# Optimization experiments

Measured on AMD Instinct MI355X. Metric: run time of the kernel, lower is better.

## Reference

```python
import jax, jax.numpy as jnp
import numpy as np

K_TOP = 2        # experts_per_tok
E_MLP = 8        # num_mlp_experts


def setup_inputs() -> dict:
    key = jax.random.key(0)
    ks = jax.random.split(key, 6)
    B, T, C, H, E_ve, V = 2, 2048, 1024, 2048, 2, 32000
    return {
        "x": jax.random.normal(ks[0], (B, T, C), dtype=jnp.float32),
        "token_ids": jax.random.randint(ks[1], (B, T), 0, V, dtype=jnp.int32),
        "w_up": jax.random.normal(ks[2], (E_MLP, H, C), dtype=jnp.float32) * 0.02,
        "w_down": jax.random.normal(ks[3], (E_MLP, C, H), dtype=jnp.float32) * 0.02,
        "router_w": jax.random.normal(ks[4], (E_MLP + E_ve, C), dtype=jnp.float32) * 0.02,
        "router_bias": jnp.zeros((E_MLP + E_ve,), dtype=jnp.float32),
        "ve_tables": jax.random.normal(ks[5], (E_ve, V, C), dtype=jnp.float32) * 0.02,
    }


def reference(x, token_ids, w_up, w_down, router_w, router_bias, ve_tables):
    B, T, C = x.shape
    N = B * T
    E_total = router_w.shape[0]
    x_flat = x.reshape(N, C)

    # Sigmoid router with aux-loss-free bias (DeepSeekV3 style): select top-k on
    # biased scores, gate with unbiased sigmoid scores normalized over the top-k.
    scores = jax.nn.sigmoid(x_flat @ router_w.T)              # (N, E_total)
    _, top_idx = jax.lax.top_k(scores + router_bias, K_TOP)   # (N, k)
    top_w = jnp.take_along_axis(scores, top_idx, axis=1)      # (N, k)
    top_w = top_w / jnp.sum(top_w, axis=1, keepdims=True)

    rows = jnp.arange(N)[:, None]
    sparse_w = jnp.zeros((N, E_total), dtype=x.dtype).at[rows, top_idx].set(top_w)

    # Dense all-expert FFN (relu^2 activation), then mask by routing weights.
    hidden = jnp.einsum('nc,ehc->enh', x_flat, w_up)          # (E_mlp, N, H)
    hidden = jnp.square(jax.nn.relu(hidden))
    mlp_out = jnp.einsum('enh,ech->enc', hidden, w_down)      # (E_mlp, N, C)
    mlp_contrib = jnp.einsum('enc,ne->nc', mlp_out, sparse_w[:, :E_MLP])

    # VE experts: shared embedding lookups, (E_ve, N, C).
    ve_out = ve_tables[:, token_ids.reshape(N), :]
    ve_contrib = jnp.einsum('enc,ne->nc', ve_out, sparse_w[:, E_MLP:])

    return (mlp_contrib + ve_contrib).reshape(B, T, C)
```

## Files before the change

kernel.cpp:

```cpp
#include <hip/hip_runtime.h>
#include <hip/hip_bf16.h>
#include <stdint.h>

#define N_TOK 4096
#define C_DIM 1024
#define H_DIM 2048
#define V_DIM 32000
#define NE_MLP 8
#define NE_TOT 10

typedef __attribute__((ext_vector_type(8))) short bf16x8;
typedef __attribute__((ext_vector_type(4))) short bf16x4;
typedef __attribute__((ext_vector_type(4))) float f32x4;

#define BM 128
#define BN 128
#define HKE 32
#define HALF_ELEMS (128 * 32)

__device__ __forceinline__ void gload16(const void* g, void* l) {
    __builtin_amdgcn_global_load_lds(
        (const __attribute__((address_space(1))) void*)g,
        (__attribute__((address_space(3))) void*)l,
        16, 0, 0);
}

__device__ __forceinline__ unsigned short bf16bits(float v) {
    __hip_bfloat16 h = __float2bfloat16(v);
    return *reinterpret_cast<unsigned short*>(&h);
}

#define CVT_N0 (N_TOK * C_DIM / 4)
#define CVT_N1 (NE_MLP * H_DIM * C_DIM / 4)
__global__ void __launch_bounds__(256) cvt_kernel(
    const float* __restrict__ x, const float* __restrict__ wu,
    const float* __restrict__ wd, __hip_bfloat16* __restrict__ xb,
    __hip_bfloat16* __restrict__ wub, __hip_bfloat16* __restrict__ wdb)
{
    const int i = blockIdx.x * 256 + threadIdx.x;
    const float* src;
    __hip_bfloat16* dst;
    int j;
    if (i < CVT_N0)            { src = x;  dst = xb;  j = i; }
    else if (i < CVT_N0 + CVT_N1) { src = wu; dst = wub; j = i - CVT_N0; }
    else                       { src = wd; dst = wdb; j = i - CVT_N0 - CVT_N1; }
    f32x4 v = reinterpret_cast<const f32x4*>(src)[j];
    bf16x4 b;
    b.x = (short)bf16bits(v.x); b.y = (short)bf16bits(v.y);
    b.z = (short)bf16bits(v.z); b.w = (short)bf16bits(v.w);
    reinterpret_cast<bf16x4*>(dst)[j] = b;
}

__global__ void __launch_bounds__(256) router_kernel(
    const float* __restrict__ x, const float* __restrict__ rw,
    const float* __restrict__ rb, int* __restrict__ tok_list,
    int* __restrict__ te, int* __restrict__ tp, float* __restrict__ tw,
    float* __restrict__ vw, int* __restrict__ cnt)
{
    const int lane = threadIdx.x & 63;
    const int n = blockIdx.x * 4 + (threadIdx.x >> 6);
    const f32x4* xr  = reinterpret_cast<const f32x4*>(x + (size_t)n * C_DIM);
    const f32x4* rw4 = reinterpret_cast<const f32x4*>(rw);

    float acc[NE_TOT];
    #pragma unroll
    for (int e = 0; e < NE_TOT; ++e) acc[e] = 0.f;

    #pragma unroll
    for (int kk = 0; kk < C_DIM / 256; ++kk) {
        f32x4 xv = xr[kk * 64 + lane];
        #pragma unroll
        for (int e = 0; e < NE_TOT; ++e) {
            f32x4 wv = rw4[e * (C_DIM / 4) + kk * 64 + lane];
            acc[e] += xv.x * wv.x + xv.y * wv.y + xv.z * wv.z + xv.w * wv.w;
        }
    }
    #pragma unroll
    for (int e = 0; e < NE_TOT; ++e) {
        for (int m = 32; m > 0; m >>= 1) acc[e] += __shfl_xor(acc[e], m, 64);
    }

    if (lane == 0) {
        float s[NE_TOT], sb[NE_TOT];
        #pragma unroll
        for (int e = 0; e < NE_TOT; ++e) {
            s[e]  = 1.f / (1.f + expf(-acc[e]));
            sb[e] = s[e] + rb[e];
        }
        int i0 = 0;
        #pragma unroll
        for (int e = 1; e < NE_TOT; ++e) if (sb[e] > sb[i0]) i0 = e;
        int i1 = (i0 == 0) ? 1 : 0;
        #pragma unroll
        for (int e = 0; e < NE_TOT; ++e)
            if (e != i0 && sb[e] > sb[i1]) i1 = e;

        float w0 = s[i0], w1 = s[i1];
        float inv = 1.f / (w0 + w1);
        w0 *= inv; w1 *= inv;

        float wv0 = 0.f, wv1 = 0.f;
        int   idx[2] = {i0, i1};
        float wt[2]  = {w0, w1};
        #pragma unroll
        for (int k = 0; k < 2; ++k) {
            if (idx[k] < NE_MLP) {
                int p = atomicAdd(&cnt[idx[k]], 1);
                tok_list[idx[k] * N_TOK + p] = n;
                te[n * 2 + k] = idx[k];
                tp[n * 2 + k] = p;
                tw[n * 2 + k] = wt[k];
            } else {
                te[n * 2 + k] = -1;
                tp[n * 2 + k] = 0;
                tw[n * 2 + k] = 0.f;
                if (idx[k] == NE_MLP) wv0 = wt[k]; else wv1 = wt[k];
            }
        }
        vw[n * 2 + 0] = wv0;
        vw[n * 2 + 1] = wv1;
    }
}

__global__ void __launch_bounds__(256) up_kernel(
    const __hip_bfloat16* __restrict__ xb, const __hip_bfloat16* __restrict__ wub,
    const int* __restrict__ tok_list, const int* __restrict__ cnt,
    __hip_bfloat16* __restrict__ hidden)
{
    const int e = blockIdx.z;
    const int count = cnt[e];
    const int m0 = blockIdx.y * BM;
    if (m0 >= count) return;
    const int n0 = blockIdx.x * BN;

    __shared__ __hip_bfloat16 lA[2 * HALF_ELEMS];
    __shared__ __hip_bfloat16 lB[2 * HALF_ELEMS];

    const int tid  = threadIdx.x;
    const int lane = tid & 63;
    const int wv   = tid >> 6;
    const int wm = (wv >> 1) * 64;
    const int wn = (wv & 1) * 64;

    const __hip_bfloat16* ga[2];
    const __hip_bfloat16* gb[2];
    __hip_bfloat16* la[2];
    __hip_bfloat16* lb[2];
    const __hip_bfloat16* wB = wub + (size_t)e * H_DIM * C_DIM;
    #pragma unroll
    for (int t = 0; t < 2; ++t) {
        const int srow = (wv + 4 * t) * 16 + (lane >> 2);
        int r = m0 + srow;
        const int tok = tok_list[e * N_TOK + (r < count ? r : count - 1)];
        ga[t] = xb + (size_t)tok * C_DIM + (lane & 3) * 8;
        gb[t] = wB + (size_t)(n0 + srow) * C_DIM + (lane & 3) * 8;
        la[t] = lA + (wv + 4 * t) * 512;
        lb[t] = lB + (wv + 4 * t) * 512;
    }

    f32x4 acc[4][4];
    #pragma unroll
    for (int i = 0; i < 4; ++i)
        #pragma unroll
        for (int j = 0; j < 4; ++j)
            acc[i][j] = (f32x4){0.f, 0.f, 0.f, 0.f};

    const int fm  = lane & 15;
    const int fkb = (lane >> 4) * 8;

    for (int k0 = 0; k0 < C_DIM; k0 += 2 * HKE) {
        __syncthreads();
        #pragma unroll
        for (int h = 0; h < 2; ++h) {
            #pragma unroll
            for (int t = 0; t < 2; ++t) {
                gload16(ga[t] + h * HKE, la[t] + h * HALF_ELEMS);
                gload16(gb[t] + h * HKE, lb[t] + h * HALF_ELEMS);
            }
        }
        #pragma unroll
        for (int t = 0; t < 2; ++t) { ga[t] += 2 * HKE; gb[t] += 2 * HKE; }
        __syncthreads();
        #pragma unroll
        for (int h = 0; h < 2; ++h) {
            bf16x8 af[4], bfr[4];
            #pragma unroll
            for (int i = 0; i < 4; ++i) {
                af[i]  = *reinterpret_cast<const bf16x8*>(lA + h * HALF_ELEMS + (wm + i * 16 + fm) * HKE + fkb);
                bfr[i] = *reinterpret_cast<const bf16x8*>(lB + h * HALF_ELEMS + (wn + i * 16 + fm) * HKE + fkb);
            }
            #pragma unroll
            for (int i = 0; i < 4; ++i)
                #pragma unroll
                for (int j = 0; j < 4; ++j)
                    acc[i][j] = __builtin_amdgcn_mfma_f32_16x16x32_bf16(af[i], bfr[j], acc[i][j], 0, 0, 0);
        }
    }

    const int fr = (lane >> 4) * 4;
    #pragma unroll
    for (int i = 0; i < 4; ++i) {
        #pragma unroll
        for (int r = 0; r < 4; ++r) {
            const int gr = m0 + wm + i * 16 + fr + r;
            const bool ok = gr < count;
            unsigned int pk[4];
            #pragma unroll
            for (int j = 0; j < 4; ++j) {
                float v = acc[i][j][r];
                v = v > 0.f ? v * v : 0.f;
                unsigned short b = bf16bits(v);
                int other = __shfl_xor((int)b, 1, 64);
                pk[j] = (unsigned)b | ((unsigned)other << 16);
            }
            if (ok && !(lane & 1)) {
                __hip_bfloat16* hrow = hidden + (size_t)(e * N_TOK + gr) * H_DIM + n0 + wn + fm;
                #pragma unroll
                for (int j = 0; j < 4; ++j)
                    *reinterpret_cast<unsigned int*>(hrow + j * 16) = pk[j];
            }
        }
    }
}

#define MLP_SLAB ((size_t)NE_MLP * N_TOK * C_DIM)
__global__ void __launch_bounds__(256) down_kernel(
    const __hip_bfloat16* __restrict__ hidden, const __hip_bfloat16* __restrict__ wdb,
    const int* __restrict__ cnt, float* __restrict__ mlp_buf)
{
    const int e  = blockIdx.z >> 1;
    const int kh = blockIdx.z & 1;
    const int count = cnt[e];
    const int m0 = blockIdx.y * BM;
    if (m0 >= count) return;
    const int n0 = blockIdx.x * BN;
    const int kbase = kh * (H_DIM / 2);

    __shared__ __hip_bfloat16 lA[2 * HALF_ELEMS];
    __shared__ __hip_bfloat16 lB[2 * HALF_ELEMS];

    const int tid  = threadIdx.x;
    const int lane = tid & 63;
    const int wv   = tid >> 6;
    const int wm = (wv >> 1) * 64;
    const int wn = (wv & 1) * 64;

    const __hip_bfloat16* ga[2];
    const __hip_bfloat16* gb[2];
    __hip_bfloat16* la[2];
    __hip_bfloat16* lb[2];
    const __hip_bfloat16* wB = wdb + (size_t)e * C_DIM * H_DIM;
    #pragma unroll
    for (int t = 0; t < 2; ++t) {
        const int srow = (wv + 4 * t) * 16 + (lane >> 2);
        int r = m0 + srow;
        const int arow = e * N_TOK + (r < count ? r : count - 1);
        ga[t] = hidden + (size_t)arow * H_DIM + kbase + (lane & 3) * 8;
        gb[t] = wB + (size_t)(n0 + srow) * H_DIM + kbase + (lane & 3) * 8;
        la[t] = lA + (wv + 4 * t) * 512;
        lb[t] = lB + (wv + 4 * t) * 512;
    }

    f32x4 acc[4][4];
    #pragma unroll
    for (int i = 0; i < 4; ++i)
        #pragma unroll
        for (int j = 0; j < 4; ++j)
            acc[i][j] = (f32x4){0.f, 0.f, 0.f, 0.f};

    const int fm  = lane & 15;
    const int fkb = (lane >> 4) * 8;

    for (int k0 = 0; k0 < H_DIM / 2; k0 += 2 * HKE) {
        __syncthreads();
        #pragma unroll
        for (int h = 0; h < 2; ++h) {
            #pragma unroll
            for (int t = 0; t < 2; ++t) {
                gload16(ga[t] + h * HKE, la[t] + h * HALF_ELEMS);
                gload16(gb[t] + h * HKE, lb[t] + h * HALF_ELEMS);
            }
        }
        #pragma unroll
        for (int t = 0; t < 2; ++t) { ga[t] += 2 * HKE; gb[t] += 2 * HKE; }
        __syncthreads();
        #pragma unroll
        for (int h = 0; h < 2; ++h) {
            bf16x8 af[4], bfr[4];
            #pragma unroll
            for (int i = 0; i < 4; ++i) {
                af[i]  = *reinterpret_cast<const bf16x8*>(lA + h * HALF_ELEMS + (wm + i * 16 + fm) * HKE + fkb);
                bfr[i] = *reinterpret_cast<const bf16x8*>(lB + h * HALF_ELEMS + (wn + i * 16 + fm) * HKE + fkb);
            }
            #pragma unroll
            for (int i = 0; i < 4; ++i)
                #pragma unroll
                for (int j = 0; j < 4; ++j)
                    acc[i][j] = __builtin_amdgcn_mfma_f32_16x16x32_bf16(af[i], bfr[j], acc[i][j], 0, 0, 0);
        }
    }

    float* obuf = mlp_buf + (size_t)kh * MLP_SLAB;
    const int fr = (lane >> 4) * 4;
    #pragma unroll
    for (int i = 0; i < 4; ++i) {
        #pragma unroll
        for (int r = 0; r < 4; ++r) {
            const int gr = m0 + wm + i * 16 + fr + r;
            if (gr < count) {
                float* orow = obuf + (size_t)(e * N_TOK + gr) * C_DIM + n0 + wn + fm;
                #pragma unroll
                for (int j = 0; j < 4; ++j)
                    orow[j * 16] = acc[i][j][r];
            }
        }
    }
}

__global__ void __launch_bounds__(256) combine_kernel(
    const int* __restrict__ token_ids, const float* __restrict__ vt,
    const float* __restrict__ vw, const int* __restrict__ te,
    const int* __restrict__ tp, const float* __restrict__ tw,
    const float* __restrict__ mlp_buf, float* __restrict__ out)
{
    const int n = blockIdx.x;
    const int c = threadIdx.x;
    const int t = token_ids[n];
    const float w0 = vw[n * 2 + 0];
    const float w1 = vw[n * 2 + 1];
    f32x4 v = {0.f, 0.f, 0.f, 0.f};
    if (w0 != 0.f)
        v += w0 * reinterpret_cast<const f32x4*>(vt + (size_t)t * C_DIM)[c];
    if (w1 != 0.f)
        v += w1 * reinterpret_cast<const f32x4*>(vt + ((size_t)V_DIM + t) * C_DIM)[c];
    #pragma unroll
    for (int k = 0; k < 2; ++k) {
        const int e = te[n * 2 + k];
        if (e >= 0) {
            const size_t slot = (size_t)(e * N_TOK + tp[n * 2 + k]) * C_DIM;
            f32x4 a = reinterpret_cast<const f32x4*>(mlp_buf + slot)[c];
            f32x4 b = reinterpret_cast<const f32x4*>(mlp_buf + MLP_SLAB + slot)[c];
            v += tw[n * 2 + k] * (a + b);
        }
    }
    reinterpret_cast<f32x4*>(out + (size_t)n * C_DIM)[c] = v;
}

extern "C" void kernel_launch(void* const* d_in, const int* in_sizes, int n_in,
                              void* d_out, int out_size, void* d_ws, size_t ws_size,
                              hipStream_t stream)
{
    const float* x         = (const float*)d_in[0];
    const int*   token_ids = (const int*)  d_in[1];
    const float* w_up      = (const float*)d_in[2];
    const float* w_down    = (const float*)d_in[3];
    const float* router_w  = (const float*)d_in[4];
    const float* router_b  = (const float*)d_in[5];
    const float* ve_tables = (const float*)d_in[6];
    float* out = (float*)d_out;

    char* ws = (char*)d_ws;
    size_t off = 0;
    __hip_bfloat16* hidden  = (__hip_bfloat16*)(ws + off); off += (size_t)NE_MLP * N_TOK * H_DIM * 2;
    float*          mlp_buf = (float*)         (ws + off); off += 2 * MLP_SLAB * 4;
    __hip_bfloat16* xb      = (__hip_bfloat16*)(ws + off); off += (size_t)N_TOK * C_DIM * 2;
    __hip_bfloat16* wub     = (__hip_bfloat16*)(ws + off); off += (size_t)NE_MLP * H_DIM * C_DIM * 2;
    __hip_bfloat16* wdb     = (__hip_bfloat16*)(ws + off); off += (size_t)NE_MLP * C_DIM * H_DIM * 2;
    int*   tok_list = (int*)  (ws + off); off += (size_t)NE_MLP * N_TOK * 4;
    int*   te       = (int*)  (ws + off); off += (size_t)N_TOK * 2 * 4;
    int*   tp       = (int*)  (ws + off); off += (size_t)N_TOK * 2 * 4;
    float* tw       = (float*)(ws + off); off += (size_t)N_TOK * 2 * 4;
    float* vw       = (float*)(ws + off); off += (size_t)N_TOK * 2 * 4;
    int*   cnt      = (int*)  (ws + off); off += 64;

    hipMemsetAsync(cnt, 0, NE_MLP * sizeof(int), stream);

    cvt_kernel<<<(CVT_N0 + 2 * CVT_N1) / 256, 256, 0, stream>>>(
        x, w_up, w_down, xb, wub, wdb);
    router_kernel<<<N_TOK / 4, 256, 0, stream>>>(x, router_w, router_b,
                                                 tok_list, te, tp, tw, vw, cnt);
    up_kernel<<<dim3(H_DIM / BN, N_TOK / BM, NE_MLP), 256, 0, stream>>>(
        xb, wub, tok_list, cnt, hidden);
    down_kernel<<<dim3(C_DIM / BN, N_TOK / BM, NE_MLP * 2), 256, 0, stream>>>(
        hidden, wdb, cnt, mlp_buf);
    combine_kernel<<<N_TOK, 256, 0, stream>>>(token_ids, ve_tables, vw,
                                              te, tp, tw, mlp_buf, out);
}
```

Before: 585.3 us.

## Fuse combine into down GEMM via atomic scatter, fold x cast into router, remap blocks

The down-projection now scales each output row by its routing weight and atomically adds it straight into the output, which the VE kernel initialises first. This removes the large fp32 mlp_buf round trip and the separate combine pass. The x-to-bf16 conversion moves into the router kernel, and the up and down grids get a swizzled block-id remap so that neighbouring blocks land on different experts and tiles. The cost is heavy atomic traffic from split-K halves and two experts per token, and fp32 summation order that is no longer deterministic.

```diff
diff --git a/kernel.cpp b/kernel.cpp
--- a/kernel.cpp
+++ b/kernel.cpp
@@ -30,20 +30,17 @@
     return *reinterpret_cast<unsigned short*>(&h);
 }
 
-#define CVT_N0 (N_TOK * C_DIM / 4)
-#define CVT_N1 (NE_MLP * H_DIM * C_DIM / 4)
+#define CVT_W (NE_MLP * H_DIM * C_DIM / 4)
 __global__ void __launch_bounds__(256) cvt_kernel(
-    const float* __restrict__ x, const float* __restrict__ wu,
-    const float* __restrict__ wd, __hip_bfloat16* __restrict__ xb,
+    const float* __restrict__ wu, const float* __restrict__ wd,
     __hip_bfloat16* __restrict__ wub, __hip_bfloat16* __restrict__ wdb)
 {
     const int i = blockIdx.x * 256 + threadIdx.x;
     const float* src;
     __hip_bfloat16* dst;
     int j;
-    if (i < CVT_N0)            { src = x;  dst = xb;  j = i; }
-    else if (i < CVT_N0 + CVT_N1) { src = wu; dst = wub; j = i - CVT_N0; }
-    else                       { src = wd; dst = wdb; j = i - CVT_N0 - CVT_N1; }
+    if (i < CVT_W) { src = wu; dst = wub; j = i; }
+    else           { src = wd; dst = wdb; j = i - CVT_W; }
     f32x4 v = reinterpret_cast<const f32x4*>(src)[j];
     bf16x4 b;
     b.x = (short)bf16bits(v.x); b.y = (short)bf16bits(v.y);
@@ -53,14 +50,15 @@
 
 __global__ void __launch_bounds__(256) router_kernel(
     const float* __restrict__ x, const float* __restrict__ rw,
-    const float* __restrict__ rb, int* __restrict__ tok_list,
-    int* __restrict__ te, int* __restrict__ tp, float* __restrict__ tw,
+    const float* __restrict__ rb, __hip_bfloat16* __restrict__ xb,
+    int* __restrict__ tok_list, float* __restrict__ wlist,
     float* __restrict__ vw, int* __restrict__ cnt)
 {
     const int lane = threadIdx.x & 63;
     const int n = blockIdx.x * 4 + (threadIdx.x >> 6);
     const f32x4* xr  = reinterpret_cast<const f32x4*>(x + (size_t)n * C_DIM);
     const f32x4* rw4 = reinterpret_cast<const f32x4*>(rw);
+    bf16x4* xbr = reinterpret_cast<bf16x4*>(xb + (size_t)n * C_DIM);
 
     float acc[NE_TOT];
     #pragma unroll
@@ -69,6 +67,10 @@
     #pragma unroll
     for (int kk = 0; kk < C_DIM / 256; ++kk) {
         f32x4 xv = xr[kk * 64 + lane];
+        bf16x4 xbv;
+        xbv.x = (short)bf16bits(xv.x); xbv.y = (short)bf16bits(xv.y);
+        xbv.z = (short)bf16bits(xv.z); xbv.w = (short)bf16bits(xv.w);
+        xbr[kk * 64 + lane] = xbv;
         #pragma unroll
         for (int e = 0; e < NE_TOT; ++e) {
             f32x4 wv = rw4[e * (C_DIM / 4) + kk * 64 + lane];
@@ -107,13 +109,8 @@
             if (idx[k] < NE_MLP) {
                 int p = atomicAdd(&cnt[idx[k]], 1);
                 tok_list[idx[k] * N_TOK + p] = n;
-                te[n * 2 + k] = idx[k];
-                tp[n * 2 + k] = p;
-                tw[n * 2 + k] = wt[k];
+                wlist[idx[k] * N_TOK + p] = wt[k];
             } else {
-                te[n * 2 + k] = -1;
-                tp[n * 2 + k] = 0;
-                tw[n * 2 + k] = 0.f;
                 if (idx[k] == NE_MLP) wv0 = wt[k]; else wv1 = wt[k];
             }
         }
@@ -122,206 +119,9 @@
     }
 }
 
-__global__ void __launch_bounds__(256) up_kernel(
-    const __hip_bfloat16* __restrict__ xb, const __hip_bfloat16* __restrict__ wub,
-    const int* __restrict__ tok_list, const int* __restrict__ cnt,
-    __hip_bfloat16* __restrict__ hidden)
-{
-    const int e = blockIdx.z;
-    const int count = cnt[e];
-    const int m0 = blockIdx.y * BM;
-    if (m0 >= count) return;
-    const int n0 = blockIdx.x * BN;
-
-    __shared__ __hip_bfloat16 lA[2 * HALF_ELEMS];
-    __shared__ __hip_bfloat16 lB[2 * HALF_ELEMS];
-
-    const int tid  = threadIdx.x;
-    const int lane = tid & 63;
-    const int wv   = tid >> 6;
-    const int wm = (wv >> 1) * 64;
-    const int wn = (wv & 1) * 64;
-
-    const __hip_bfloat16* ga[2];
-    const __hip_bfloat16* gb[2];
-    __hip_bfloat16* la[2];
-    __hip_bfloat16* lb[2];
-    const __hip_bfloat16* wB = wub + (size_t)e * H_DIM * C_DIM;
-    #pragma unroll
-    for (int t = 0; t < 2; ++t) {
-        const int srow = (wv + 4 * t) * 16 + (lane >> 2);
-        int r = m0 + srow;
-        const int tok = tok_list[e * N_TOK + (r < count ? r : count - 1)];
-        ga[t] = xb + (size_t)tok * C_DIM + (lane & 3) * 8;
-        gb[t] = wB + (size_t)(n0 + srow) * C_DIM + (lane & 3) * 8;
-        la[t] = lA + (wv + 4 * t) * 512;
-        lb[t] = lB + (wv + 4 * t) * 512;
-    }
-
-    f32x4 acc[4][4];
-    #pragma unroll
-    for (int i = 0; i < 4; ++i)
-        #pragma unroll
-        for (int j = 0; j < 4; ++j)
-            acc[i][j] = (f32x4){0.f, 0.f, 0.f, 0.f};
-
-    const int fm  = lane & 15;
-    const int fkb = (lane >> 4) * 8;
-
-    for (int k0 = 0; k0 < C_DIM; k0 += 2 * HKE) {
-        __syncthreads();
-        #pragma unroll
-        for (int h = 0; h < 2; ++h) {
-            #pragma unroll
-            for (int t = 0; t < 2; ++t) {
-                gload16(ga[t] + h * HKE, la[t] + h * HALF_ELEMS);
-                gload16(gb[t] + h * HKE, lb[t] + h * HALF_ELEMS);
-            }
-        }
-        #pragma unroll
-        for (int t = 0; t < 2; ++t) { ga[t] += 2 * HKE; gb[t] += 2 * HKE; }
-        __syncthreads();
-        #pragma unroll
-        for (int h = 0; h < 2; ++h) {
-            bf16x8 af[4], bfr[4];
-            #pragma unroll
-            for (int i = 0; i < 4; ++i) {
-                af[i]  = *reinterpret_cast<const bf16x8*>(lA + h * HALF_ELEMS + (wm + i * 16 + fm) * HKE + fkb);
-                bfr[i] = *reinterpret_cast<const bf16x8*>(lB + h * HALF_ELEMS + (wn + i * 16 + fm) * HKE + fkb);
-            }
-            #pragma unroll
-            for (int i = 0; i < 4; ++i)
-                #pragma unroll
-                for (int j = 0; j < 4; ++j)
-                    acc[i][j] = __builtin_amdgcn_mfma_f32_16x16x32_bf16(af[i], bfr[j], acc[i][j], 0, 0, 0);
-        }
-    }
-
-    const int fr = (lane >> 4) * 4;
-    #pragma unroll
-    for (int i = 0; i < 4; ++i) {
-        #pragma unroll
-        for (int r = 0; r < 4; ++r) {
-            const int gr = m0 + wm + i * 16 + fr + r;
-            const bool ok = gr < count;
-            unsigned int pk[4];
-            #pragma unroll
-            for (int j = 0; j < 4; ++j) {
-                float v = acc[i][j][r];
-                v = v > 0.f ? v * v : 0.f;
-                unsigned short b = bf16bits(v);
-                int other = __shfl_xor((int)b, 1, 64);
-                pk[j] = (unsigned)b | ((unsigned)other << 16);
-            }
-            if (ok && !(lane & 1)) {
-                __hip_bfloat16* hrow = hidden + (size_t)(e * N_TOK + gr) * H_DIM + n0 + wn + fm;
-                #pragma unroll
-                for (int j = 0; j < 4; ++j)
-                    *reinterpret_cast<unsigned int*>(hrow + j * 16) = pk[j];
-            }
-        }
-    }
-}
-
-#define MLP_SLAB ((size_t)NE_MLP * N_TOK * C_DIM)
-__global__ void __launch_bounds__(256) down_kernel(
-    const __hip_bfloat16* __restrict__ hidden, const __hip_bfloat16* __restrict__ wdb,
-    const int* __restrict__ cnt, float* __restrict__ mlp_buf)
-{
-    const int e  = blockIdx.z >> 1;
-    const int kh = blockIdx.z & 1;
-    const int count = cnt[e];
-    const int m0 = blockIdx.y * BM;
-    if (m0 >= count) return;
-    const int n0 = blockIdx.x * BN;
-    const int kbase = kh * (H_DIM / 2);
-
-    __shared__ __hip_bfloat16 lA[2 * HALF_ELEMS];
-    __shared__ __hip_bfloat16 lB[2 * HALF_ELEMS];
-
-    const int tid  = threadIdx.x;
-    const int lane = tid & 63;
-    const int wv   = tid >> 6;
-    const int wm = (wv >> 1) * 64;
-    const int wn = (wv & 1) * 64;
-
-    const __hip_bfloat16* ga[2];
-    const __hip_bfloat16* gb[2];
-    __hip_bfloat16* la[2];
-    __hip_bfloat16* lb[2];
-    const __hip_bfloat16* wB = wdb + (size_t)e * C_DIM * H_DIM;
-    #pragma unroll
-    for (int t = 0; t < 2; ++t) {
-        const int srow = (wv + 4 * t) * 16 + (lane >> 2);
-        int r = m0 + srow;
-        const int arow = e * N_TOK + (r < count ? r : count - 1);
-        ga[t] = hidden + (size_t)arow * H_DIM + kbase + (lane & 3) * 8;
-        gb[t] = wB + (size_t)(n0 + srow) * H_DIM + kbase + (lane & 3) * 8;
-        la[t] = lA + (wv + 4 * t) * 512;
-        lb[t] = lB + (wv + 4 * t) * 512;
-    }
-
-    f32x4 acc[4][4];
-    #pragma unroll
-    for (int i = 0; i < 4; ++i)
-        #pragma unroll
-        for (int j = 0; j < 4; ++j)
-            acc[i][j] = (f32x4){0.f, 0.f, 0.f, 0.f};
-
-    const int fm  = lane & 15;
-    const int fkb = (lane >> 4) * 8;
-
-    for (int k0 = 0; k0 < H_DIM / 2; k0 += 2 * HKE) {
-        __syncthreads();
-        #pragma unroll
-        for (int h = 0; h < 2; ++h) {
-            #pragma unroll
-            for (int t = 0; t < 2; ++t) {
-                gload16(ga[t] + h * HKE, la[t] + h * HALF_ELEMS);
-                gload16(gb[t] + h * HKE, lb[t] + h * HALF_ELEMS);
-            }
-        }
-        #pragma unroll
-        for (int t = 0; t < 2; ++t) { ga[t] += 2 * HKE; gb[t] += 2 * HKE; }
-        __syncthreads();
-        #pragma unroll
-        for (int h = 0; h < 2; ++h) {
-            bf16x8 af[4], bfr[4];
-            #pragma unroll
-            for (int i = 0; i < 4; ++i) {
-                af[i]  = *reinterpret_cast<const bf16x8*>(lA + h * HALF_ELEMS + (wm + i * 16 + fm) * HKE + fkb);
-                bfr[i] = *reinterpret_cast<const bf16x8*>(lB + h * HALF_ELEMS + (wn + i * 16 + fm) * HKE + fkb);
-            }
-            #pragma unroll
-            for (int i = 0; i < 4; ++i)
-                #pragma unroll
-                for (int j = 0; j < 4; ++j)
-                    acc[i][j] = __builtin_amdgcn_mfma_f32_16x16x32_bf16(af[i], bfr[j], acc[i][j], 0, 0, 0);
-        }
-    }
-
-    float* obuf = mlp_buf + (size_t)kh * MLP_SLAB;
-    const int fr = (lane >> 4) * 4;
-    #pragma unroll
-    for (int i = 0; i < 4; ++i) {
-        #pragma unroll
-        for (int r = 0; r < 4; ++r) {
-            const int gr = m0 + wm + i * 16 + fr + r;
-            if (gr < count) {
-                float* orow = obuf + (size_t)(e * N_TOK + gr) * C_DIM + n0 + wn + fm;
-                #pragma unroll
-                for (int j = 0; j < 4; ++j)
-                    orow[j * 16] = acc[i][j][r];
-            }
-        }
-    }
-}
-
-__global__ void __launch_bounds__(256) combine_kernel(
+__global__ void __launch_bounds__(256) ve_kernel(
     const int* __restrict__ token_ids, const float* __restrict__ vt,
-    const float* __restrict__ vw, const int* __restrict__ te,
-    const int* __restrict__ tp, const float* __restrict__ tw,
-    const float* __restrict__ mlp_buf, float* __restrict__ out)
+    const float* __restrict__ vw, float* __restrict__ out)
 {
     const int n = blockIdx.x;
     const int c = threadIdx.x;
@@ -333,17 +133,212 @@
         v += w0 * reinterpret_cast<const f32x4*>(vt + (size_t)t * C_DIM)[c];
     if (w1 != 0.f)
         v += w1 * reinterpret_cast<const f32x4*>(vt + ((size_t)V_DIM + t) * C_DIM)[c];
-    #pragma unroll
-    for (int k = 0; k < 2; ++k) {
-        const int e = te[n * 2 + k];
-        if (e >= 0) {
-            const size_t slot = (size_t)(e * N_TOK + tp[n * 2 + k]) * C_DIM;
-            f32x4 a = reinterpret_cast<const f32x4*>(mlp_buf + slot)[c];
-            f32x4 b = reinterpret_cast<const f32x4*>(mlp_buf + MLP_SLAB + slot)[c];
-            v += tw[n * 2 + k] * (a + b);
-        }
-    }
     reinterpret_cast<f32x4*>(out + (size_t)n * C_DIM)[c] = v;
+}
+
+__global__ void __launch_bounds__(256) up_kernel(
+    const __hip_bfloat16* __restrict__ xb, const __hip_bfloat16* __restrict__ wub,
+    const int* __restrict__ tok_list, const int* __restrict__ cnt,
+    __hip_bfloat16* __restrict__ hidden)
+{
+    const int lid = (blockIdx.z * 32 + blockIdx.y) * 16 + blockIdx.x;
+    const int s   = (lid & 7) * 512 + (lid >> 3);
+    const int bx = s & 15, by = (s >> 4) & 31, bz = s >> 9;
+
+    const int e = bz;
+    const int count = cnt[e];
+    const int m0 = by * BM;
+    if (m0 >= count) return;
+    const int n0 = bx * BN;
+
+    __shared__ __hip_bfloat16 lA[2 * HALF_ELEMS];
+    __shared__ __hip_bfloat16 lB[2 * HALF_ELEMS];
+
+    const int tid  = threadIdx.x;
+    const int lane = tid & 63;
+    const int wv   = tid >> 6;
+    const int wm = (wv >> 1) * 64;
+    const int wn = (wv & 1) * 64;
+
+    const __hip_bfloat16* ga[2];
+    const __hip_bfloat16* gb[2];
+    __hip_bfloat16* la[2];
+    __hip_bfloat16* lb[2];
+    const __hip_bfloat16* wB = wub + (size_t)e * H_DIM * C_DIM;
+    #pragma unroll
+    for (int t = 0; t < 2; ++t) {
+        const int srow = (wv + 4 * t) * 16 + (lane >> 2);
+        int r = m0 + srow;
+        const int tok = tok_list[e * N_TOK + (r < count ? r : count - 1)];
+        ga[t] = xb + (size_t)tok * C_DIM + (lane & 3) * 8;
+        gb[t] = wB + (size_t)(n0 + srow) * C_DIM + (lane & 3) * 8;
+        la[t] = lA + (wv + 4 * t) * 512;
+        lb[t] = lB + (wv + 4 * t) * 512;
+    }
+
+    f32x4 acc[4][4];
+    #pragma unroll
+    for (int i = 0; i < 4; ++i)
+        #pragma unroll
+        for (int j = 0; j < 4; ++j)
+            acc[i][j] = (f32x4){0.f, 0.f, 0.f, 0.f};
+
+    const int fm  = lane & 15;
+    const int fkb = (lane >> 4) * 8;
+
+    for (int k0 = 0; k0 < C_DIM; k0 += 2 * HKE) {
+        __syncthreads();
+        #pragma unroll
+        for (int h = 0; h < 2; ++h) {
+            #pragma unroll
+            for (int t = 0; t < 2; ++t) {
+                gload16(ga[t] + h * HKE, la[t] + h * HALF_ELEMS);
+                gload16(gb[t] + h * HKE, lb[t] + h * HALF_ELEMS);
+            }
+        }
+        #pragma unroll
+        for (int t = 0; t < 2; ++t) { ga[t] += 2 * HKE; gb[t] += 2 * HKE; }
+        __syncthreads();
+        #pragma unroll
+        for (int h = 0; h < 2; ++h) {
+            bf16x8 af[4], bfr[4];
+            #pragma unroll
+            for (int i = 0; i < 4; ++i) {
+                af[i]  = *reinterpret_cast<const bf16x8*>(lA + h * HALF_ELEMS + (wm + i * 16 + fm) * HKE + fkb);
+                bfr[i] = *reinterpret_cast<const bf16x8*>(lB + h * HALF_ELEMS + (wn + i * 16 + fm) * HKE + fkb);
+            }
+            #pragma unroll
+            for (int i = 0; i < 4; ++i)
+                #pragma unroll
+                for (int j = 0; j < 4; ++j)
+                    acc[i][j] = __builtin_amdgcn_mfma_f32_16x16x32_bf16(af[i], bfr[j], acc[i][j], 0, 0, 0);
+        }
+    }
+
+    const int fr = (lane >> 4) * 4;
+    #pragma unroll
+    for (int i = 0; i < 4; ++i) {
+        #pragma unroll
+        for (int r = 0; r < 4; ++r) {
+            const int gr = m0 + wm + i * 16 + fr + r;
+            const bool ok = gr < count;
+            unsigned int pk[4];
+            #pragma unroll
+            for (int j = 0; j < 4; ++j) {
+                float v = acc[i][j][r];
+                v = v > 0.f ? v * v : 0.f;
+                unsigned short b = bf16bits(v);
+                int other = __shfl_xor((int)b, 1, 64);
+                pk[j] = (unsigned)b | ((unsigned)other << 16);
+            }
+            if (ok && !(lane & 1)) {
+                __hip_bfloat16* hrow = hidden + (size_t)(e * N_TOK + gr) * H_DIM + n0 + wn + fm;
+                #pragma unroll
+                for (int j = 0; j < 4; ++j)
+                    *reinterpret_cast<unsigned int*>(hrow + j * 16) = pk[j];
+            }
+        }
+    }
+}
+
+__global__ void __launch_bounds__(256) down_kernel(
+    const __hip_bfloat16* __restrict__ hidden, const __hip_bfloat16* __restrict__ wdb,
+    const int* __restrict__ tok_list, const float* __restrict__ wlist,
+    const int* __restrict__ cnt, float* __restrict__ out)
+{
+    const int lid = (blockIdx.z * 32 + blockIdx.y) * 8 + blockIdx.x;
+    const int s   = (lid & 7) * 512 + (lid >> 3);
+    const int bx = s & 7, by = (s >> 3) & 31, bz = s >> 8;
+
+    const int e  = bz >> 1;
+    const int kh = bz & 1;
+    const int count = cnt[e];
+    const int m0 = by * BM;
+    if (m0 >= count) return;
+    const int n0 = bx * BN;
+    const int kbase = kh * (H_DIM / 2);
+
+    __shared__ __hip_bfloat16 lA[2 * HALF_ELEMS];
+    __shared__ __hip_bfloat16 lB[2 * HALF_ELEMS];
+
+    const int tid  = threadIdx.x;
+    const int lane = tid & 63;
+    const int wv   = tid >> 6;
+    const int wm = (wv >> 1) * 64;
+    const int wn = (wv & 1) * 64;
+
+    const __hip_bfloat16* ga[2];
+    const __hip_bfloat16* gb[2];
+    __hip_bfloat16* la[2];
+    __hip_bfloat16* lb[2];
+    const __hip_bfloat16* wB = wdb + (size_t)e * C_DIM * H_DIM;
+    #pragma unroll
+    for (int t = 0; t < 2; ++t) {
+        const int srow = (wv + 4 * t) * 16 + (lane >> 2);
+        int r = m0 + srow;
+        const int arow = e * N_TOK + (r < count ? r : count - 1);
+        ga[t] = hidden + (size_t)arow * H_DIM + kbase + (lane & 3) * 8;
+        gb[t] = wB + (size_t)(n0 + srow) * H_DIM + kbase + (lane & 3) * 8;
+        la[t] = lA + (wv + 4 * t) * 512;
+        lb[t] = lB + (wv + 4 * t) * 512;
+    }
+
+    f32x4 acc[4][4];
+    #pragma unroll
+    for (int i = 0; i < 4; ++i)
+        #pragma unroll
+        for (int j = 0; j < 4; ++j)
+            acc[i][j] = (f32x4){0.f, 0.f, 0.f, 0.f};
+
+    const int fm  = lane & 15;
+    const int fkb = (lane >> 4) * 8;
+
+    for (int k0 = 0; k0 < H_DIM / 2; k0 += 2 * HKE) {
+        __syncthreads();
+        #pragma unroll
+        for (int h = 0; h < 2; ++h) {
+            #pragma unroll
+            for (int t = 0; t < 2; ++t) {
+                gload16(ga[t] + h * HKE, la[t] + h * HALF_ELEMS);
+                gload16(gb[t] + h * HKE, lb[t] + h * HALF_ELEMS);
+            }
+        }
+        #pragma unroll
+        for (int t = 0; t < 2; ++t) { ga[t] += 2 * HKE; gb[t] += 2 * HKE; }
+        __syncthreads();
+        #pragma unroll
+        for (int h = 0; h < 2; ++h) {
+            bf16x8 af[4], bfr[4];
+            #pragma unroll
+            for (int i = 0; i < 4; ++i) {
+                af[i]  = *reinterpret_cast<const bf16x8*>(lA + h * HALF_ELEMS + (wm + i * 16 + fm) * HKE + fkb);
+                bfr[i] = *reinterpret_cast<const bf16x8*>(lB + h * HALF_ELEMS + (wn + i * 16 + fm) * HKE + fkb);
+            }
+            #pragma unroll
+            for (int i = 0; i < 4; ++i)
+                #pragma unroll
+                for (int j = 0; j < 4; ++j)
+                    acc[i][j] = __builtin_amdgcn_mfma_f32_16x16x32_bf16(af[i], bfr[j], acc[i][j], 0, 0, 0);
+        }
+    }
+
+    const int fr = (lane >> 4) * 4;
+    #pragma unroll
+    for (int i = 0; i < 4; ++i) {
+        #pragma unroll
+        for (int r = 0; r < 4; ++r) {
+            const int gr = m0 + wm + i * 16 + fr + r;
+            if (gr < count) {
+                const int   tok = tok_list[e * N_TOK + gr];
+                const float w   = wlist[e * N_TOK + gr];
+                float* orow = out + (size_t)tok * C_DIM + n0 + wn + fm;
+                #pragma unroll
+                for (int j = 0; j < 4; ++j)
+                    __hip_atomic_fetch_add(orow + j * 16, w * acc[i][j][r],
+                                           __ATOMIC_RELAXED, __HIP_MEMORY_SCOPE_AGENT);
+            }
+        }
+    }
 }
 
 extern "C" void kernel_launch(void* const* d_in, const int* in_sizes, int n_in,
@@ -362,27 +357,22 @@
     char* ws = (char*)d_ws;
     size_t off = 0;
     __hip_bfloat16* hidden  = (__hip_bfloat16*)(ws + off); off += (size_t)NE_MLP * N_TOK * H_DIM * 2;
-    float*          mlp_buf = (float*)         (ws + off); off += 2 * MLP_SLAB * 4;
     __hip_bfloat16* xb      = (__hip_bfloat16*)(ws + off); off += (size_t)N_TOK * C_DIM * 2;
     __hip_bfloat16* wub     = (__hip_bfloat16*)(ws + off); off += (size_t)NE_MLP * H_DIM * C_DIM * 2;
     __hip_bfloat16* wdb     = (__hip_bfloat16*)(ws + off); off += (size_t)NE_MLP * C_DIM * H_DIM * 2;
     int*   tok_list = (int*)  (ws + off); off += (size_t)NE_MLP * N_TOK * 4;
-    int*   te       = (int*)  (ws + off); off += (size_t)N_TOK * 2 * 4;
-    int*   tp       = (int*)  (ws + off); off += (size_t)N_TOK * 2 * 4;
-    float* tw       = (float*)(ws + off); off += (size_t)N_TOK * 2 * 4;
+    float* wlist    = (float*)(ws + off); off += (size_t)NE_MLP * N_TOK * 4;
     float* vw       = (float*)(ws + off); off += (size_t)N_TOK * 2 * 4;
     int*   cnt      = (int*)  (ws + off); off += 64;
 
     hipMemsetAsync(cnt, 0, NE_MLP * sizeof(int), stream);
 
-    cvt_kernel<<<(CVT_N0 + 2 * CVT_N1) / 256, 256, 0, stream>>>(
-        x, w_up, w_down, xb, wub, wdb);
-    router_kernel<<<N_TOK / 4, 256, 0, stream>>>(x, router_w, router_b,
-                                                 tok_list, te, tp, tw, vw, cnt);
+    router_kernel<<<N_TOK / 4, 256, 0, stream>>>(x, router_w, router_b, xb,
+                                                 tok_list, wlist, vw, cnt);
+    cvt_kernel<<<2 * CVT_W / 256, 256, 0, stream>>>(w_up, w_down, wub, wdb);
+    ve_kernel<<<N_TOK, 256, 0, stream>>>(token_ids, ve_tables, vw, out);
     up_kernel<<<dim3(H_DIM / BN, N_TOK / BM, NE_MLP), 256, 0, stream>>>(
         xb, wub, tok_list, cnt, hidden);
     down_kernel<<<dim3(C_DIM / BN, N_TOK / BM, NE_MLP * 2), 256, 0, stream>>>(
-        hidden, wdb, cnt, mlp_buf);
-    combine_kernel<<<N_TOK, 256, 0, stream>>>(token_ids, ve_tables, vw,
-                                              te, tp, tw, mlp_buf, out);
-}
+        hidden, wdb, tok_list, wlist, cnt, out);
+}
```

Result: no change. 596.3 us (+1.9%).
